# Performance work log

Measured on AMD Instinct MI355X. Metric: run time of the kernel, lower is better.

The kernel has to match this reference:

```python
import jax, jax.numpy as jnp
import numpy as np

SUB_NO = 64
SYN_BASIS_NO = 3
T_HIST = 200
T_DATA = 100000


def setup_inputs() -> dict:
    key = jax.random.key(0)
    ks = jax.random.split(key, 5)
    # strictly-lower-triangular adjacency: each subunit integrates from ancestors
    C_den = jnp.tril((jax.random.uniform(ks[0], (SUB_NO, SUB_NO)) < 0.15).astype(jnp.float32), k=-1)
    S_conv = jax.random.normal(ks[1], (T_DATA, SUB_NO), dtype=jnp.float32)
    Y_ancest = 0.1 * jax.random.normal(ks[2], (T_DATA, SUB_NO), dtype=jnp.float32)
    # sparse binary spike trains
    Z_ancest = (jax.random.uniform(ks[3], (T_DATA, SUB_NO)) < 0.05).astype(jnp.float32)
    V_o = jnp.full((1,), -69.0, dtype=jnp.float32)
    W_sub = jnp.full((SUB_NO,), 0.25, dtype=jnp.float32)
    theta_syn = jnp.zeros((SUB_NO,), dtype=jnp.float32)
    K_spike = jnp.full((SUB_NO, SYN_BASIS_NO), 0.01, dtype=jnp.float32)
    tau_spike = jnp.arange(1.6, 1.6 + SYN_BASIS_NO, dtype=jnp.float32)
    delta_spike = jnp.zeros((SUB_NO,), dtype=jnp.float32)
    return {"S_conv": S_conv, "Y_ancest": Y_ancest, "Z_ancest": Z_ancest,
            "C_den": C_den, "V_o": V_o, "W_sub": W_sub, "theta_syn": theta_syn,
            "K_spike": K_spike, "tau_spike": tau_spike, "delta_spike": delta_spike,
            "T_hist": T_HIST}


def _ancest_kernel(K_spike, tau_spike, delta_spike, T_hist):
    # t[s, k] = max(k - delta_s, 0); kern[s, k] = sum_b (t/tau_b) exp(-t/tau_b) K[s,b]
    t = jnp.arange(T_hist, dtype=jnp.float32)[None, :] - delta_spike[:, None]
    t = jnp.maximum(t, 0.0)                                  # [sub, T_hist]
    tau = jnp.exp(tau_spike)                                 # [basis]
    t_tau = t[:, None, :] / tau[None, :, None]               # [sub, basis, T_hist]
    kern = jnp.sum(t_tau * jnp.exp(-t_tau) * K_spike[:, :, None], axis=1)
    return kern                                              # [sub, T_hist]


def reference(S_conv, Y_ancest, Z_ancest, C_den, V_o, W_sub, theta_syn,
              K_spike, tau_spike, delta_spike, T_hist):
    T_data, sub_no = S_conv.shape
    kern = _ancest_kernel(K_spike, tau_spike, delta_spike, T_hist)
    kern_f = jnp.flip(kern, axis=1)                          # matches torch.flip

    # spike_ancest[t, s, k] = sum_j C_den[s,j] Z_pad[t+k, j]  ->  precontract once
    Zc = Z_ancest @ C_den.T                                  # [T, sub]
    Zc_pad = jnp.concatenate([jnp.zeros((T_hist, sub_no), Zc.dtype), Zc], axis=0)
    # depthwise VALID conv over time: filtered[t, s] = sum_k kern_f[s,k] Zc_pad[t+k, s]
    out = jax.lax.conv_general_dilated(
        Zc_pad.T[None],                                      # [1, sub, T+T_hist]
        kern_f[:, None, :],                                  # [sub, 1, T_hist]
        window_strides=(1,), padding='VALID',
        feature_group_count=sub_no,
        dimension_numbers=('NCH', 'OIH', 'NCH'))
    filtered = out[0, :, :T_data].T                          # [T, sub]

    raw = Y_ancest @ C_den.T                                 # [T, sub]
    X_in = S_conv + theta_syn + filtered + raw
    final_Y = jax.nn.sigmoid(X_in) * W_sub + V_o
    return final_Y
```

## Files before the change

### kernel.cpp

```cpp
#include <hip/hip_runtime.h>

#define SUBS  64
#define GUARD 256
#define NCH   32
#define OCH   28
#define RW    32
#define RB    (RW * 4)

typedef _Float16 f16x8 __attribute__((ext_vector_type(8)));
typedef float    f32x4 __attribute__((ext_vector_type(4)));

__device__ inline f16x8 ld_frag(const float* p) {
    float4 a = *(const float4*)p;
    float4 b = *(const float4*)(p + 4);
    f16x8 f;
    f[0]=(_Float16)a.x; f[1]=(_Float16)a.y; f[2]=(_Float16)a.z; f[3]=(_Float16)a.w;
    f[4]=(_Float16)b.x; f[5]=(_Float16)b.y; f[6]=(_Float16)b.z; f[7]=(_Float16)b.w;
    return f;
}
__device__ inline uint pkh2(float a, float b) {
    union { _Float16 h[2]; uint u; } p;
    p.h[0] = (_Float16)a; p.h[1] = (_Float16)b; return p.u;
}

__global__ __launch_bounds__(256, 4) void k_mm(
    const float* __restrict__ Z, const float* __restrict__ Y,
    const float* __restrict__ C,
    _Float16* __restrict__ Zt, _Float16* __restrict__ Yt, int T, int TS)
{
    __shared__ _Float16 ztl[SUBS * 136];
    __shared__ _Float16 ytl[SUBS * 136];
    const int tid  = threadIdx.x;
    const int lane = tid & 63;
    const int wv   = tid >> 6;
    const int lr   = lane & 15;
    const int lg   = lane >> 4;
    const int t0b  = blockIdx.x * 128;

    if (blockIdx.x < 8) {
        const int chunk = blockIdx.x * 256 + tid;
        const int s = chunk >> 5;
        const int c = (chunk & 31) * 8;
        uint4 z4 = {0, 0, 0, 0};
        *(uint4*)&Zt[(size_t)s * TS + c] = z4;
    }

    f16x8 bfr[4][2];
    #pragma unroll
    for (int nt = 0; nt < 4; ++nt)
        #pragma unroll
        for (int ks = 0; ks < 2; ++ks)
            bfr[nt][ks] = ld_frag(&C[(lr + 16 * nt) * 64 + ks * 32 + lg * 8]);

    #pragma unroll
    for (int g = 0; g < 2; ++g) {
        const int t0 = t0b + wv * 32 + g * 16;
        const int rowA = t0 + lr;
        const bool okA = rowA < T;
        f16x8 az[2], ay[2];
        #pragma unroll
        for (int ks = 0; ks < 2; ++ks) {
            if (okA) {
                az[ks] = ld_frag(&Z[(size_t)rowA * 64 + ks * 32 + lg * 8]);
                ay[ks] = ld_frag(&Y[(size_t)rowA * 64 + ks * 32 + lg * 8]);
            } else {
                az[ks] = (f16x8)(_Float16)0.f;
                ay[ks] = (f16x8)(_Float16)0.f;
            }
        }

        f32x4 accZ[4], accY[4];
        #pragma unroll
        for (int nt = 0; nt < 4; ++nt) { accZ[nt] = (f32x4){0,0,0,0}; accY[nt] = (f32x4){0,0,0,0}; }
        #pragma unroll
        for (int nt = 0; nt < 4; ++nt) {
            #pragma unroll
            for (int ks = 0; ks < 2; ++ks) {
                accZ[nt] = __builtin_amdgcn_mfma_f32_16x16x32_f16(az[ks], bfr[nt][ks], accZ[nt], 0, 0, 0);
                accY[nt] = __builtin_amdgcn_mfma_f32_16x16x32_f16(ay[ks], bfr[nt][ks], accY[nt], 0, 0, 0);
            }
        }

        #pragma unroll
        for (int nt = 0; nt < 4; ++nt) {
            const int sc = lr + 16 * nt;
            const int lt = wv * 32 + g * 16 + lg * 4;
            uint2 pz, py;
            pz.x = pkh2(accZ[nt][0], accZ[nt][1]);
            pz.y = pkh2(accZ[nt][2], accZ[nt][3]);
            py.x = pkh2(accY[nt][0], accY[nt][1]);
            py.y = pkh2(accY[nt][2], accY[nt][3]);
            *(uint2*)&ztl[sc * 136 + lt] = pz;
            *(uint2*)&ytl[sc * 136 + lt] = py;
        }
    }

    __syncthreads();

    #pragma unroll
    for (int it = 0; it < 4; ++it) {
        const int chunk = tid + it * 256;
        const int row = chunk >> 4;
        const int col = chunk & 15;
        const int tb  = t0b + col * 8;
        const uint4 vz = *(const uint4*)&ztl[row * 136 + col * 8];
        const uint4 vy = *(const uint4*)&ytl[row * 136 + col * 8];
        if (tb + 7 < T) {
            *(uint4*)&Zt[(size_t)row * TS + GUARD + tb] = vz;
            *(uint4*)&Yt[(size_t)row * TS + GUARD + tb] = vy;
        } else {
            #pragma unroll
            for (int h = 0; h < 8; ++h)
                if (tb + h < T) {
                    Zt[(size_t)row * TS + GUARD + tb + h] = ztl[row * 136 + col * 8 + h];
                    Yt[(size_t)row * TS + GUARD + tb + h] = ytl[row * 136 + col * 8 + h];
                }
        }
    }
}

#define SEL4(cur, nxt0, sel)                                                     \
    sel[0] = off ? __builtin_amdgcn_alignbit((cur).y, (cur).x, 16) : (cur).x;    \
    sel[1] = off ? __builtin_amdgcn_alignbit((cur).z, (cur).y, 16) : (cur).y;    \
    sel[2] = off ? __builtin_amdgcn_alignbit((cur).w, (cur).z, 16) : (cur).z;    \
    sel[3] = off ? __builtin_amdgcn_alignbit((nxt0),  (cur).w, 16) : (cur).w;

#define STEP3(u)                                                                 \
    _Pragma("unroll")                                                            \
    for (int b = 0; b < 3; ++b) {                                                \
        const float yn = fmaf(twr[b], y1[b], fmaf(mr2[b], y2[b], cr[b] * (u)));  \
        y2[b] = y1[b]; y1[b] = yn;                                               \
    }

#define CHUNK8(cur, nxt0)                                                        \
    {                                                                            \
        uint sel[4];                                                             \
        SEL4(cur, nxt0, sel);                                                    \
        _Pragma("unroll")                                                        \
        for (int i = 0; i < 4; ++i) {                                            \
            union { uint u; _Float16 h[2]; } w; w.u = sel[i];                    \
            STEP3((float)w.h[0]);                                                \
            STEP3((float)w.h[1]);                                                \
        }                                                                        \
    }

__global__ __launch_bounds__(256, 3) void k_iir(
    const _Float16* __restrict__ Zt, const _Float16* __restrict__ Yt,
    const float* __restrict__ S,
    const float* __restrict__ K_spike, const float* __restrict__ tau_spike,
    const float* __restrict__ delta_spike, const float* __restrict__ theta,
    const float* __restrict__ W, const float* __restrict__ Vo,
    float* __restrict__ out, int T, int TS)
{
    const int tid = threadIdx.x;
    const int s   = tid & 63;
    const int wv  = tid >> 6;
    const int t0  = blockIdx.x * RB + wv * RW;
    if (t0 >= T) return;

    float twr[3], mr2[3], cr[3];
    #pragma unroll
    for (int b = 0; b < 3; ++b) {
        const float tau = __expf(tau_spike[b]);
        const float r   = __expf(-1.0f / tau);
        twr[b] = 2.0f * r;
        mr2[b] = -r * r;
        cr[b]  = K_spike[s * 3 + b] / tau * r;
    }
    int dl = (int)rintf(delta_spike[s]);
    dl = min(max(dl, 0), 30);

    const int xi0 = t0 - 8 * NCH + RW - 2 - dl;
    const int xb0 = xi0 & ~1;
    const uint off = (uint)(xi0 & 1);

    const _Float16* rowp = Zt + (size_t)s * TS + GUARD;
    const uint4* xp = (const uint4*)(rowp + xb0);

    uint4 yv[4];
    {
        const uint4* yp = (const uint4*)(Yt + (size_t)s * TS + GUARD + t0);
        #pragma unroll
        for (int p = 0; p < 4; ++p) yv[p] = yp[p];
    }
    float sreg[RW];
    #pragma unroll
    for (int o = 0; o < RW; ++o) {
        const int tt = min(t0 + o, T - 1);
        sreg[o] = S[(size_t)tt * 64 + s];
    }

    uint4 buf[8];
    #pragma unroll
    for (int p = 0; p < 8; ++p) buf[p] = xp[p];

    float y1[3] = {0.f, 0.f, 0.f}, y2[3] = {0.f, 0.f, 0.f};

    #pragma unroll 1
    for (int cc = 0; cc < 3; ++cc) {
        #pragma unroll
        for (int j = 0; j < 8; ++j) {
            const int c = cc * 8 + j;
            const uint4 cur  = buf[j];
            const uint  nxt0 = buf[(j + 1) & 7].x;
            buf[j] = xp[c + 8];
            __builtin_amdgcn_sched_barrier(0);
            CHUNK8(cur, nxt0);
        }
    }
    #pragma unroll
    for (int j = 0; j < 4; ++j) {
        const uint4 cur  = buf[j];
        const uint  nxt0 = buf[j + 1].x;
        CHUNK8(cur, nxt0);
    }

    const float wsub = W[s];
    const float vo   = Vo[0];
    const float th   = theta[s];
    #pragma unroll
    for (int j = 4; j < 8; ++j) {
        const uint4 cur  = buf[j];
        const uint  nxt0 = (j < 7) ? buf[j + 1].x : 0u;
        uint sel[4];
        SEL4(cur, nxt0, sel);
        union { uint4 v; _Float16 h[8]; } yw;
        yw.v = yv[j - 4];
        #pragma unroll
        for (int i = 0; i < 4; ++i) {
            union { uint u; _Float16 h[2]; } w; w.u = sel[i];
            #pragma unroll
            for (int hh = 0; hh < 2; ++hh) {
                STEP3((float)w.h[hh]);
                const int o = (j - 4) * 8 + i * 2 + hh;
                const int t = t0 + o;
                if (t < T) {
                    const float xin = (float)yw.h[i * 2 + hh] + sreg[o] + th
                                      + y1[0] + y1[1] + y1[2];
                    const float sig = 1.0f / (1.0f + __expf(-xin));
                    out[(size_t)t * 64 + s] = fmaf(sig, wsub, vo);
                }
            }
        }
    }
}

extern "C" void kernel_launch(void* const* d_in, const int* in_sizes, int n_in,
                              void* d_out, int out_size, void* d_ws, size_t ws_size,
                              hipStream_t stream)
{
    const float* S     = (const float*)d_in[0];
    const float* Y     = (const float*)d_in[1];
    const float* Z     = (const float*)d_in[2];
    const float* C     = (const float*)d_in[3];
    const float* Vo    = (const float*)d_in[4];
    const float* W     = (const float*)d_in[5];
    const float* theta = (const float*)d_in[6];
    const float* K     = (const float*)d_in[7];
    const float* tau   = (const float*)d_in[8];
    const float* delta = (const float*)d_in[9];
    const int T  = in_sizes[0] / SUBS;
    const int TS = T + GUARD;

    _Float16* Zt = (_Float16*)d_ws;
    _Float16* Yt = (_Float16*)((char*)d_ws + (size_t)SUBS * TS * 2);

    k_mm<<<(T + 127) / 128, 256, 0, stream>>>(Z, Y, C, Zt, Yt, T, TS);
    k_iir<<<(T + RB - 1) / RB, 256, 0, stream>>>(Zt, Yt, S, K, tau, delta, theta,
                                                 W, Vo, (float*)d_out, T, TS);
}
```

Before: 57.02 us.

## Tile intermediates time-major in 8-step chunks and widen IIR output windows

The fp16 intermediate buffers change from subunit-major rows to tiles of 8 timesteps × 64 subunits. Each lane's uint4 loads in the IIR kernel therefore become coalesced across subunits instead of strided per row. The output window per wave grows from 32 to 48 steps with a 224-step warm-up, so warm-up work is spread over more outputs. A fast path for zero delay drops the alignbit shifting, and a scalar fallback handles nonzero delays. Packing S+theta to fp16 lowers precision slightly, and the wider window raises register pressure.

```diff
diff --git a/kernel.cpp b/kernel.cpp
--- a/kernel.cpp
+++ b/kernel.cpp
@@ -2,10 +2,11 @@
 
 #define SUBS  64
 #define GUARD 256
-#define NCH   32
-#define OCH   28
-#define RW    32
+#define NCH   34
+#define WU    224
+#define RW    48
 #define RB    (RW * 4)
+#define LSTR  136
 
 typedef _Float16 f16x8 __attribute__((ext_vector_type(8)));
 typedef float    f32x4 __attribute__((ext_vector_type(4)));
@@ -26,10 +27,10 @@
 __global__ __launch_bounds__(256, 4) void k_mm(
     const float* __restrict__ Z, const float* __restrict__ Y,
     const float* __restrict__ C,
-    _Float16* __restrict__ Zt, _Float16* __restrict__ Yt, int T, int TS)
+    _Float16* __restrict__ Zt, _Float16* __restrict__ Yt, int T, int rgz)
 {
-    __shared__ _Float16 ztl[SUBS * 136];
-    __shared__ _Float16 ytl[SUBS * 136];
+    __shared__ _Float16 ztl[SUBS * LSTR];
+    __shared__ _Float16 ytl[SUBS * LSTR];
     const int tid  = threadIdx.x;
     const int lane = tid & 63;
     const int wv   = tid >> 6;
@@ -38,11 +39,15 @@
     const int t0b  = blockIdx.x * 128;
 
     if (blockIdx.x < 8) {
-        const int chunk = blockIdx.x * 256 + tid;
-        const int s = chunk >> 5;
-        const int c = (chunk & 31) * 8;
+        const int tile = blockIdx.x * 4 + (tid >> 6);
         uint4 z4 = {0, 0, 0, 0};
-        *(uint4*)&Zt[(size_t)s * TS + c] = z4;
+        ((uint4*)Zt)[(size_t)tile * 64 + (tid & 63)] = z4;
+        ((uint4*)Yt)[(size_t)tile * 64 + (tid & 63)] = z4;
+    } else if (blockIdx.x < 18) {
+        const int tile = rgz + (blockIdx.x - 8) * 4 + (tid >> 6);
+        uint4 z4 = {0, 0, 0, 0};
+        ((uint4*)Zt)[(size_t)tile * 64 + (tid & 63)] = z4;
+        ((uint4*)Yt)[(size_t)tile * 64 + (tid & 63)] = z4;
     }
 
     f16x8 bfr[4][2];
@@ -90,40 +95,35 @@
             pz.y = pkh2(accZ[nt][2], accZ[nt][3]);
             py.x = pkh2(accY[nt][0], accY[nt][1]);
             py.y = pkh2(accY[nt][2], accY[nt][3]);
-            *(uint2*)&ztl[sc * 136 + lt] = pz;
-            *(uint2*)&ytl[sc * 136 + lt] = py;
+            *(uint2*)&ztl[sc * LSTR + lt] = pz;
+            *(uint2*)&ytl[sc * LSTR + lt] = py;
         }
     }
 
     __syncthreads();
 
+    const int gbase = (GUARD >> 3) + blockIdx.x * 16;
     #pragma unroll
     for (int it = 0; it < 4; ++it) {
-        const int chunk = tid + it * 256;
-        const int row = chunk >> 4;
-        const int col = chunk & 15;
+        const int chunk = it * 256 + tid;
+        const int row = chunk & 63;
+        const int col = chunk >> 6;
         const int tb  = t0b + col * 8;
-        const uint4 vz = *(const uint4*)&ztl[row * 136 + col * 8];
-        const uint4 vy = *(const uint4*)&ytl[row * 136 + col * 8];
         if (tb + 7 < T) {
-            *(uint4*)&Zt[(size_t)row * TS + GUARD + tb] = vz;
-            *(uint4*)&Yt[(size_t)row * TS + GUARD + tb] = vy;
+            ((uint4*)Zt)[(size_t)(gbase + col) * 64 + row] =
+                *(const uint4*)&ztl[row * LSTR + col * 8];
+            ((uint4*)Yt)[(size_t)(gbase + col) * 64 + row] =
+                *(const uint4*)&ytl[row * LSTR + col * 8];
         } else {
             #pragma unroll
             for (int h = 0; h < 8; ++h)
                 if (tb + h < T) {
-                    Zt[(size_t)row * TS + GUARD + tb + h] = ztl[row * 136 + col * 8 + h];
-                    Yt[(size_t)row * TS + GUARD + tb + h] = ytl[row * 136 + col * 8 + h];
+                    Zt[(size_t)(gbase + col) * 512 + row * 8 + h] = ztl[row * LSTR + col * 8 + h];
+                    Yt[(size_t)(gbase + col) * 512 + row * 8 + h] = ytl[row * LSTR + col * 8 + h];
                 }
         }
     }
 }
-
-#define SEL4(cur, nxt0, sel)                                                     \
-    sel[0] = off ? __builtin_amdgcn_alignbit((cur).y, (cur).x, 16) : (cur).x;    \
-    sel[1] = off ? __builtin_amdgcn_alignbit((cur).z, (cur).y, 16) : (cur).y;    \
-    sel[2] = off ? __builtin_amdgcn_alignbit((cur).w, (cur).z, 16) : (cur).z;    \
-    sel[3] = off ? __builtin_amdgcn_alignbit((nxt0),  (cur).w, 16) : (cur).w;
 
 #define STEP3(u)                                                                 \
     _Pragma("unroll")                                                            \
@@ -132,17 +132,13 @@
         y2[b] = y1[b]; y1[b] = yn;                                               \
     }
 
-#define CHUNK8(cur, nxt0)                                                        \
-    {                                                                            \
-        uint sel[4];                                                             \
-        SEL4(cur, nxt0, sel);                                                    \
-        _Pragma("unroll")                                                        \
-        for (int i = 0; i < 4; ++i) {                                            \
-            union { uint u; _Float16 h[2]; } w; w.u = sel[i];                    \
-            STEP3((float)w.h[0]);                                                \
-            STEP3((float)w.h[1]);                                                \
-        }                                                                        \
-    }
+#define PAIRW(wrd) {                                                             \
+    union { uint u; _Float16 h[2]; } w_; w_.u = (wrd);                           \
+    STEP3((float)w_.h[0]);                                                       \
+    STEP3((float)w_.h[1]); }
+
+#define CHUNK8F(cur, nxt) {                                                      \
+    PAIRW((cur).w); PAIRW((nxt).x); PAIRW((nxt).y); PAIRW((nxt).z); }
 
 __global__ __launch_bounds__(256, 3) void k_iir(
     const _Float16* __restrict__ Zt, const _Float16* __restrict__ Yt,
@@ -150,7 +146,7 @@
     const float* __restrict__ K_spike, const float* __restrict__ tau_spike,
     const float* __restrict__ delta_spike, const float* __restrict__ theta,
     const float* __restrict__ W, const float* __restrict__ Vo,
-    float* __restrict__ out, int T, int TS)
+    float* __restrict__ out, int T)
 {
     const int tid = threadIdx.x;
     const int s   = tid & 63;
@@ -169,73 +165,93 @@
     }
     int dl = (int)rintf(delta_spike[s]);
     dl = min(max(dl, 0), 30);
-
-    const int xi0 = t0 - 8 * NCH + RW - 2 - dl;
-    const int xb0 = xi0 & ~1;
-    const uint off = (uint)(xi0 & 1);
-
-    const _Float16* rowp = Zt + (size_t)s * TS + GUARD;
-    const uint4* xp = (const uint4*)(rowp + xb0);
-
-    uint4 yv[4];
-    {
-        const uint4* yp = (const uint4*)(Yt + (size_t)s * TS + GUARD + t0);
-        #pragma unroll
-        for (int p = 0; p < 4; ++p) yv[p] = yp[p];
-    }
-    float sreg[RW];
-    #pragma unroll
-    for (int o = 0; o < RW; ++o) {
-        const int tt = min(t0 + o, T - 1);
-        sreg[o] = S[(size_t)tt * 64 + s];
-    }
-
-    uint4 buf[8];
-    #pragma unroll
-    for (int p = 0; p < 8; ++p) buf[p] = xp[p];
-
-    float y1[3] = {0.f, 0.f, 0.f}, y2[3] = {0.f, 0.f, 0.f};
-
-    #pragma unroll 1
-    for (int cc = 0; cc < 3; ++cc) {
-        #pragma unroll
-        for (int j = 0; j < 8; ++j) {
-            const int c = cc * 8 + j;
-            const uint4 cur  = buf[j];
-            const uint  nxt0 = buf[(j + 1) & 7].x;
-            buf[j] = xp[c + 8];
-            __builtin_amdgcn_sched_barrier(0);
-            CHUNK8(cur, nxt0);
-        }
-    }
-    #pragma unroll
-    for (int j = 0; j < 4; ++j) {
-        const uint4 cur  = buf[j];
-        const uint  nxt0 = buf[j + 1].x;
-        CHUNK8(cur, nxt0);
-    }
-
+    const float th   = theta[s];
     const float wsub = W[s];
     const float vo   = Vo[0];
-    const float th   = theta[s];
-    #pragma unroll
-    for (int j = 4; j < 8; ++j) {
-        const uint4 cur  = buf[j];
-        const uint  nxt0 = (j < 7) ? buf[j + 1].x : 0u;
-        uint sel[4];
-        SEL4(cur, nxt0, sel);
-        union { uint4 v; _Float16 h[8]; } yw;
-        yw.v = yv[j - 4];
-        #pragma unroll
-        for (int i = 0; i < 4; ++i) {
-            union { uint u; _Float16 h[2]; } w; w.u = sel[i];
-            #pragma unroll
-            for (int hh = 0; hh < 2; ++hh) {
-                STEP3((float)w.h[hh]);
-                const int o = (j - 4) * 8 + i * 2 + hh;
+
+    float y1[3] = {0.f, 0.f, 0.f}, y2[3] = {0.f, 0.f, 0.f};
+
+    if (__all(dl == 0)) {
+        const int tile0 = (GUARD + t0 - 232) >> 3;
+        const uint4* xb = (const uint4*)Zt + (size_t)tile0 * 64 + s;
+
+        uint4 buf[8];
+        #pragma unroll
+        for (int p = 0; p < 8; ++p) buf[p] = xb[(size_t)p * 64];
+
+        #pragma unroll 1
+        for (int cc = 0; cc < 3; ++cc) {
+            #pragma unroll
+            for (int j = 0; j < 8; ++j) {
+                const int c = cc * 8 + j;
+                const uint4 cur = buf[j];
+                const uint4 nxt = buf[(j + 1) & 7];
+                buf[j] = xb[(size_t)(c + 8) * 64];
+                __builtin_amdgcn_sched_barrier(0);
+                CHUNK8F(cur, nxt);
+            }
+        }
+
+        uint4 t32 = xb[(size_t)32 * 64];
+        uint4 t33 = xb[(size_t)33 * 64];
+        uint4 t34 = xb[(size_t)34 * 64];
+        const uint4* yb = (const uint4*)Yt + (size_t)((GUARD + t0) >> 3) * 64 + s;
+        uint4 yv[6];
+        #pragma unroll
+        for (int p = 0; p < 6; ++p) yv[p] = yb[(size_t)p * 64];
+        uint spk[24];
+        #pragma unroll
+        for (int p = 0; p < 24; ++p) {
+            const int t1 = min(t0 + 2 * p,     T - 1);
+            const int t2 = min(t0 + 2 * p + 1, T - 1);
+            spk[p] = pkh2(S[(size_t)t1 * 64 + s] + th, S[(size_t)t2 * 64 + s] + th);
+        }
+
+        #pragma unroll
+        for (int j = 0; j < 4; ++j) { CHUNK8F(buf[j], buf[j + 1]); }
+
+        #pragma unroll
+        for (int oc = 0; oc < 6; ++oc) {
+            uint4 cur, nxt;
+            if      (oc == 0) { cur = buf[4]; nxt = buf[5]; }
+            else if (oc == 1) { cur = buf[5]; nxt = buf[6]; }
+            else if (oc == 2) { cur = buf[6]; nxt = buf[7]; }
+            else if (oc == 3) { cur = buf[7]; nxt = t32;    }
+            else if (oc == 4) { cur = t32;    nxt = t33;    }
+            else              { cur = t33;    nxt = t34;    }
+            const uint sw[4] = { cur.w, nxt.x, nxt.y, nxt.z };
+            union { uint4 v; _Float16 h[8]; } yw; yw.v = yv[oc];
+            #pragma unroll
+            for (int i = 0; i < 4; ++i) {
+                union { uint u; _Float16 h[2]; } w; w.u = sw[i];
+                #pragma unroll
+                for (int hh = 0; hh < 2; ++hh) {
+                    STEP3((float)w.h[hh]);
+                    const int o = oc * 8 + i * 2 + hh;
+                    const int t = t0 + o;
+                    if (t < T) {
+                        union { uint u; _Float16 h[2]; } sp; sp.u = spk[o >> 1];
+                        const float xin = (float)yw.h[i * 2 + hh] + (float)sp.h[o & 1]
+                                          + y1[0] + y1[1] + y1[2];
+                        const float sig = 1.0f / (1.0f + __expf(-xin));
+                        out[(size_t)t * 64 + s] = fmaf(sig, wsub, vo);
+                    }
+                }
+            }
+        }
+    } else {
+        const int xi0 = t0 - 226 - dl;
+        for (int k = 0; k < 8 * NCH; ++k) {
+            const int h = GUARD + xi0 + k;
+            const float u = (float)Zt[(size_t)(h >> 3) * 512 + s * 8 + (h & 7)];
+            STEP3(u);
+            const int o = k - WU;
+            if (o >= 0) {
                 const int t = t0 + o;
                 if (t < T) {
-                    const float xin = (float)yw.h[i * 2 + hh] + sreg[o] + th
+                    const int hy = GUARD + t;
+                    const float yc = (float)Yt[(size_t)(hy >> 3) * 512 + s * 8 + (hy & 7)];
+                    const float xin = yc + S[(size_t)t * 64 + s] + th
                                       + y1[0] + y1[1] + y1[2];
                     const float sig = 1.0f / (1.0f + __expf(-xin));
                     out[(size_t)t * 64 + s] = fmaf(sig, wsub, vo);
@@ -259,13 +275,14 @@
     const float* K     = (const float*)d_in[7];
     const float* tau   = (const float*)d_in[8];
     const float* delta = (const float*)d_in[9];
-    const int T  = in_sizes[0] / SUBS;
-    const int TS = T + GUARD;
-
+    const int T = in_sizes[0] / SUBS;
+
+    const int rgz    = (GUARD + T + 7) >> 3;
+    const int ntiles = rgz + 44;
     _Float16* Zt = (_Float16*)d_ws;
-    _Float16* Yt = (_Float16*)((char*)d_ws + (size_t)SUBS * TS * 2);
-
-    k_mm<<<(T + 127) / 128, 256, 0, stream>>>(Z, Y, C, Zt, Yt, T, TS);
+    _Float16* Yt = (_Float16*)((char*)d_ws + (size_t)ntiles * 1024);
+
+    k_mm<<<(T + 127) / 128, 256, 0, stream>>>(Z, Y, C, Zt, Yt, T, rgz);
     k_iir<<<(T + RB - 1) / RB, 256, 0, stream>>>(Zt, Yt, S, K, tau, delta, theta,
-                                                 W, Vo, (float*)d_out, T, TS);
-}
+                                                 W, Vo, (float*)d_out, T);
+}
```

After: 56.31 us. About the same (-1.3%).
